# Kernel optimization log

Measured on AMD Instinct MI355X. Metric: run time of the kernel, lower is better.

## Reference

```python
import jax, jax.numpy as jnp
import numpy as np
from jax import lax

N, C, M = 512, 81, 28
NMS_THRESH = 0.5
EPS = 1e-4


def setup_inputs() -> dict:
    key = jax.random.key(0)
    k1, k2, k3, k4 = jax.random.split(key, 4)
    return {
        "left_logits": jax.random.normal(k1, (N, C, M, M), dtype=jnp.float32),
        "right_logits": jax.random.normal(k2, (N, C, M, M), dtype=jnp.float32),
        "scores": jax.random.uniform(k3, (N,), dtype=jnp.float32),
        "labels": jax.random.randint(k4, (N,), 0, C),
    }


def mask_nms_keep(probs, scores, thresh):
    # probs: [N, M, M] float mask probabilities; greedy suppression in score order.
    n = probs.shape[0]
    order = jnp.argsort(-scores)
    P = probs[order].reshape(n, -1)                  # [N, M*M] sorted by score desc
    inter = P @ P.T                                   # pairwise sum(mask_i * mask_j)
    u = P.sum(-1)                                     # per-mask area (numerator mask only)
    iou = inter / (u[:, None] + EPS)                  # asymmetric IoU as in mask_iou()
    upper = jnp.triu(jnp.ones((n, n), dtype=bool), 1) # j > i

    def body(i, suppressed):
        sup_row = (~suppressed[i]) & upper[i] & (iou[i] >= thresh)
        return suppressed | sup_row

    suppressed = lax.fori_loop(0, n, body, jnp.zeros(n, dtype=bool))
    keep_sorted = ~suppressed
    # map back to original detection order
    return jnp.zeros(n, dtype=bool).at[order].set(keep_sorted)


def reference(left_logits, right_logits, scores, labels):
    idx = jnp.arange(left_logits.shape[0])
    # full-tensor sigmoid then per-class gather, as in the original module
    left_prob = jax.nn.sigmoid(left_logits)[idx, labels][:, None]    # [N,1,M,M]
    right_prob = jax.nn.sigmoid(right_logits)[idx, labels][:, None]  # [N,1,M,M]

    # filter_empty: both sides must have nonzero mask mass
    valid = (left_prob[:, 0].sum((-1, -2)) > 0) & (right_prob[:, 0].sum((-1, -2)) > 0)

    left_keep = mask_nms_keep(left_prob[:, 0], scores, NMS_THRESH)
    right_keep = mask_nms_keep(right_prob[:, 0], scores, NMS_THRESH)
    keep = valid & left_keep & right_keep  # intersection of left/right NMS keeps

    probs = jnp.stack([left_prob, right_prob], axis=0)  # [2,N,1,M,M]
    return probs, keep
```

## Files before the change

### kernel.cpp

```cpp
#include <hip/hip_runtime.h>
#include <math.h>

#define NDET 512
#define NCLS 81
#define MM   784
#define PROBS_ELEMS (2 * NDET * MM)
#define NMS_TH 0.5
#define EPS_D  1e-4
#define SDD 114


__global__ __launch_bounds__(256) void k12_fused(
    const float* __restrict__ left, const float* __restrict__ right,
    const float* __restrict__ scores, const int* __restrict__ labels,
    float* __restrict__ out, double* __restrict__ u, int* __restrict__ order) {
  if (blockIdx.x == 256) {
    __shared__ float sk[NDET];
    __shared__ int   si[NDET];
    int t = threadIdx.x;
    for (int e = t; e < NDET; e += 256) { sk[e] = scores[e]; si[e] = e; }
    __syncthreads();
    for (int k = 2; k <= NDET; k <<= 1) {
      for (int j = k >> 1; j > 0; j >>= 1) {
        for (int e = t; e < NDET; e += 256) {
          int p = e ^ j;
          if (p > e) {
            bool dir = ((e & k) == 0);
            float sa = sk[e], sb = sk[p];
            int ia = si[e], ib = si[p];
            bool aBeforeB = (sa > sb) || (sa == sb && ia < ib);
            bool doSwap = dir ? (!aBeforeB) : aBeforeB;
            if (doSwap) { sk[e] = sb; si[e] = ib; sk[p] = sa; si[p] = ia; }
          }
        }
        __syncthreads();
      }
    }
    for (int e = t; e < NDET; e += 256) order[e] = si[e];
    return;
  }

  int wv = threadIdx.x >> 6;
  int lane = threadIdx.x & 63;
  int m = (blockIdx.x << 2) | wv;
  int s = m >> 9;
  int n = m & 511;
  const float* src = (s == 0) ? left : right;
  int lab = labels[n];
  const float4* in4 = (const float4*)(src + ((size_t)n * NCLS + lab) * MM);
  float4* out4 = (float4*)(out + ((size_t)s * NDET + n) * MM);
  double local = 0.0;
  for (int i = lane; i < MM / 4; i += 64) {
    float4 v = in4[i];
    float4 r;
    r.x = 1.0f / (1.0f + expf(-v.x));
    r.y = 1.0f / (1.0f + expf(-v.y));
    r.z = 1.0f / (1.0f + expf(-v.z));
    r.w = 1.0f / (1.0f + expf(-v.w));
    out4[i] = r;
    local += (double)r.x + (double)r.y + (double)r.z + (double)r.w;
  }
#pragma unroll
  for (int off = 32; off > 0; off >>= 1)
    local += __shfl_down(local, off, 64);
  if (lane == 0) u[s * NDET + n] = local;
}

__global__ __launch_bounds__(256, 2) void k3_iou(
    const float* __restrict__ P,
    const double* __restrict__ u,
    const int* __restrict__ order,
    unsigned int* __restrict__ bits32) {
  int bi = blockIdx.x;
  int s = bi / 136;
  int tri = bi % 136;
  int ti = 0, rem = tri;
  while (rem >= 16 - ti) { rem -= 16 - ti; ti++; }
  int tj = ti + rem;

  __shared__ __align__(16) double arena[2 * 32 * SDD];
  double (*Asd)[SDD] = (double (*)[SDD])arena;
  double (*Bsd)[SDD] = (double (*)[SDD])(arena + 32 * SDD);
  double (*Cp)[33]   = (double (*)[33])arena;
  __shared__ int oi[32], oj[32];
  __shared__ double den05[32];
  __shared__ unsigned char pred[32][32];

  int t = threadIdx.x;
  if (t < 32) {
    int r = order[ti * 32 + t];
    oi[t] = r;
    den05[t] = 0.5 * (u[s * NDET + r] + EPS_D);
    oj[t] = order[tj * 32 + t];
  }
  __syncthreads();

  const float* Pside = P + (size_t)s * NDET * MM;

  const float4* gsrc[7];
  double* ldst[7];
#pragma unroll
  for (int i = 0; i < 7; i++) {
    int idx = t + 256 * i;
    int ab = (idx >= 896);
    int idc = ab ? (idx - 896) : idx;
    int r = idc / 28;
    int c4 = idc - r * 28;
    int o = ab ? oj[r] : oi[r];
    gsrc[i] = (const float4*)(Pside + (size_t)o * MM) + c4;
    ldst[i] = ab ? &Bsd[r][4 * c4] : &Asd[r][4 * c4];
  }

  float4 pf[7];
#pragma unroll
  for (int i = 0; i < 7; i++) pf[i] = gsrc[i][0];

  int wv = t >> 6;
  int lane = t & 63;
  int tx = lane & 7;
  int ty = (lane >> 3) & 7;
  int kb = 28 * wv;

  double acc[4][4];
#pragma unroll
  for (int i = 0; i < 4; i++)
#pragma unroll
    for (int j = 0; j < 4; j++) acc[i][j] = 0.0;

  for (int kc = 0; kc < 7; kc++) {
#pragma unroll
    for (int i = 0; i < 7; i++) {
      float4 v = pf[i];
      double2 d0; d0.x = (double)v.x; d0.y = (double)v.y;
      double2 d1; d1.x = (double)v.z; d1.y = (double)v.w;
      *(double2*)(ldst[i])     = d0;
      *(double2*)(ldst[i] + 2) = d1;
    }
    __syncthreads();
    if (kc < 6) {
#pragma unroll
      for (int i = 0; i < 7; i++) pf[i] = gsrc[i][(kc + 1) * 28];
    }
#pragma unroll
    for (int kp = 0; kp < 14; kp++) {
      double2 av[4], bv[4];
#pragma unroll
      for (int i = 0; i < 4; i++)
        av[i] = *(const double2*)&Asd[ty + 8 * i][kb + 2 * kp];
#pragma unroll
      for (int j = 0; j < 4; j++)
        bv[j] = *(const double2*)&Bsd[tx + 8 * j][kb + 2 * kp];
#pragma unroll
      for (int i = 0; i < 4; i++)
#pragma unroll
        for (int j = 0; j < 4; j++) {
          acc[i][j] = fma(av[i].x, bv[j].x, acc[i][j]);
          acc[i][j] = fma(av[i].y, bv[j].y, acc[i][j]);
        }
    }
    __syncthreads();
  }

  if (wv > 0) {
#pragma unroll
    for (int i = 0; i < 4; i++)
#pragma unroll
      for (int j = 0; j < 4; j++)
        Cp[(wv - 1) * 32 + ty + 8 * i][tx + 8 * j] = acc[i][j];
  }
  __syncthreads();
  if (wv == 0) {
#pragma unroll
    for (int i = 0; i < 4; i++) {
      int r = ty + 8 * i;
#pragma unroll
      for (int j = 0; j < 4; j++) {
        int c = tx + 8 * j;
        double v = acc[i][j] + Cp[0 * 32 + r][c] + Cp[1 * 32 + r][c] +
                   Cp[2 * 32 + r][c];
        pred[r][c] = (v >= den05[r]) ? 1 : 0;
      }
    }
  }
  __syncthreads();
  if (t < 32) {
    unsigned m = 0;
#pragma unroll
    for (int c = 0; c < 32; c++) m |= ((unsigned)pred[t][c]) << c;
    bits32[((size_t)s * NDET + ti * 32 + t) * 16 + tj] = m;
  }
}

__global__ __launch_bounds__(512) void k4_greedy(
    const unsigned long long* __restrict__ bits,
    const int* __restrict__ order,
    const double* __restrict__ u,
    float* __restrict__ outKeep) {
  __shared__ unsigned long long B[2 * NDET * 8];
  __shared__ unsigned char keepO[2 * NDET];
  int t = threadIdx.x;

  for (int e = t; e < 2 * NDET * 8; e += 512) {
    unsigned long long w = bits[e];
    int g = e & 7;
    int i = (e >> 3) & 511;
    int gi = i >> 6;
    if (g < gi) {
      w = 0ull;
    } else if (g == gi) {
      int li = i & 63;
      w = (li == 63) ? 0ull : (w & (~0ull << (li + 1)));
    }
    B[e] = w;
  }
  __syncthreads();

  int wv = t >> 6;
  int lane = t & 63;
  if (wv < 2) {
    int s = wv;
    const unsigned long long* Bside = B + (size_t)s * NDET * 8;
    unsigned long long S0 = 0, S1 = 0, S2 = 0, S3 = 0,
                       S4 = 0, S5 = 0, S6 = 0, S7 = 0;

#define GROUP(G, SG, ORS)                                              \
    for (int li = 0; li < 64; li++) {                                  \
      unsigned act = (unsigned)((SG >> li) & 1ull);                    \
      if (__builtin_amdgcn_readfirstlane(act) == 0) {                  \
        const unsigned long long* row = Bside + ((((G) << 6) | li) << 3); \
        ORS                                                            \
      }                                                                \
    }
    GROUP(0, S0, { S0 |= row[0]; S1 |= row[1]; S2 |= row[2]; S3 |= row[3];
                   S4 |= row[4]; S5 |= row[5]; S6 |= row[6]; S7 |= row[7]; })
    GROUP(1, S1, { S1 |= row[1]; S2 |= row[2]; S3 |= row[3];
                   S4 |= row[4]; S5 |= row[5]; S6 |= row[6]; S7 |= row[7]; })
    GROUP(2, S2, { S2 |= row[2]; S3 |= row[3];
                   S4 |= row[4]; S5 |= row[5]; S6 |= row[6]; S7 |= row[7]; })
    GROUP(3, S3, { S3 |= row[3];
                   S4 |= row[4]; S5 |= row[5]; S6 |= row[6]; S7 |= row[7]; })
    GROUP(4, S4, { S4 |= row[4]; S5 |= row[5]; S6 |= row[6]; S7 |= row[7]; })
    GROUP(5, S5, { S5 |= row[5]; S6 |= row[6]; S7 |= row[7]; })
    GROUP(6, S6, { S6 |= row[6]; S7 |= row[7]; })
    GROUP(7, S7, { S7 |= row[7]; })
#undef GROUP

    unsigned long long Sarr[8] = {S0, S1, S2, S3, S4, S5, S6, S7};
#pragma unroll
    for (int g = 0; g < 8; g++) {
      int c = (g << 6) | lane;
      keepO[s * NDET + order[c]] =
          (unsigned char)(((Sarr[g] >> lane) & 1ull) ^ 1ull);
    }
  }
  __syncthreads();

  if (t < NDET) {
    bool valid = (u[t] > 0.0) && (u[NDET + t] > 0.0);
    outKeep[t] = (valid && keepO[t] && keepO[NDET + t]) ? 1.0f : 0.0f;
  }
}

extern "C" void kernel_launch(void* const* d_in, const int* in_sizes, int n_in,
                              void* d_out, int out_size, void* d_ws, size_t ws_size,
                              hipStream_t stream) {
  const float* left   = (const float*)d_in[0];
  const float* right  = (const float*)d_in[1];
  const float* scores = (const float*)d_in[2];
  const int*   labels = (const int*)d_in[3];
  float* out = (float*)d_out;

  char* ws = (char*)d_ws;
  double* u                = (double*)(ws + 0);
  int* order               = (int*)(ws + 8192);
  unsigned int* bits32     = (unsigned int*)(ws + 16384);
  unsigned long long* bits = (unsigned long long*)(ws + 16384);

  k12_fused<<<257, 256, 0, stream>>>(left, right, scores, labels, out, u, order);
  k3_iou<<<272, 256, 0, stream>>>(out, u, order, bits32);
  k4_greedy<<<1, 512, 0, stream>>>(bits, order, u, out + PROBS_ELEMS);
}
```

Before: 281.7 us.

## Fuse greedy NMS into IoU kernel via last-block atomic counter; retile accumulators

```diff
diff --git a/kernel.cpp b/kernel.cpp
--- a/kernel.cpp
+++ b/kernel.cpp
@@ -13,11 +13,13 @@
 __global__ __launch_bounds__(256) void k12_fused(
     const float* __restrict__ left, const float* __restrict__ right,
     const float* __restrict__ scores, const int* __restrict__ labels,
-    float* __restrict__ out, double* __restrict__ u, int* __restrict__ order) {
+    float* __restrict__ out, double* __restrict__ u, int* __restrict__ order,
+    int* counter) {
   if (blockIdx.x == 256) {
     __shared__ float sk[NDET];
     __shared__ int   si[NDET];
     int t = threadIdx.x;
+    if (t == 0 && counter) *counter = 0;
     for (int e = t; e < NDET; e += 256) { sk[e] = scores[e]; si[e] = e; }
     __syncthreads();
     for (int k = 2; k <= NDET; k <<= 1) {
@@ -66,11 +68,20 @@
   if (lane == 0) u[s * NDET + n] = local;
 }
 
+__device__ __forceinline__ unsigned long long diagmask(unsigned long long w,
+                                                       int g, int gi, int li) {
+  if (g < gi) return 0ull;
+  if (g == gi) return (li == 63) ? 0ull : (w & (~0ull << (li + 1)));
+  return w;
+}
+
 __global__ __launch_bounds__(256, 2) void k3_iou(
     const float* __restrict__ P,
     const double* __restrict__ u,
     const int* __restrict__ order,
-    unsigned int* __restrict__ bits32) {
+    unsigned int* bits32,
+    float* __restrict__ outKeep,
+    int* counter, int fused) {
   int bi = blockIdx.x;
   int s = bi / 136;
   int tri = bi % 136;
@@ -78,13 +89,15 @@
   while (rem >= 16 - ti) { rem -= 16 - ti; ti++; }
   int tj = ti + rem;
 
-  __shared__ __align__(16) double arena[2 * 32 * SDD];
+  __shared__ __align__(16) double arena[8192];
   double (*Asd)[SDD] = (double (*)[SDD])arena;
   double (*Bsd)[SDD] = (double (*)[SDD])(arena + 32 * SDD);
   double (*Cp)[33]   = (double (*)[33])arena;
   __shared__ int oi[32], oj[32];
   __shared__ double den05[32];
   __shared__ unsigned char pred[32][32];
+  __shared__ unsigned char keepO[2 * NDET];
+  __shared__ int lastFlag;
 
   int t = threadIdx.x;
   if (t < 32) {
@@ -117,15 +130,16 @@
 
   int wv = t >> 6;
   int lane = t & 63;
-  int tx = lane & 7;
-  int ty = (lane >> 3) & 7;
-  int kb = 28 * wv;
-
-  double acc[4][4];
+  int tx = lane & 3;
+  int ty = (lane >> 2) & 7;
+  int kg = lane >> 5;
+  int kb = 14 * (wv * 2 + kg);
+
+  double acc[4][8];
 #pragma unroll
   for (int i = 0; i < 4; i++)
 #pragma unroll
-    for (int j = 0; j < 4; j++) acc[i][j] = 0.0;
+    for (int j = 0; j < 8; j++) acc[i][j] = 0.0;
 
   for (int kc = 0; kc < 7; kc++) {
 #pragma unroll
@@ -142,18 +156,18 @@
       for (int i = 0; i < 7; i++) pf[i] = gsrc[i][(kc + 1) * 28];
     }
 #pragma unroll
-    for (int kp = 0; kp < 14; kp++) {
-      double2 av[4], bv[4];
+    for (int kp = 0; kp < 7; kp++) {
+      double2 av[4], bv[8];
 #pragma unroll
       for (int i = 0; i < 4; i++)
         av[i] = *(const double2*)&Asd[ty + 8 * i][kb + 2 * kp];
 #pragma unroll
-      for (int j = 0; j < 4; j++)
-        bv[j] = *(const double2*)&Bsd[tx + 8 * j][kb + 2 * kp];
+      for (int j = 0; j < 8; j++)
+        bv[j] = *(const double2*)&Bsd[tx + 4 * j][kb + 2 * kp];
 #pragma unroll
       for (int i = 0; i < 4; i++)
 #pragma unroll
-        for (int j = 0; j < 4; j++) {
+        for (int j = 0; j < 8; j++) {
           acc[i][j] = fma(av[i].x, bv[j].x, acc[i][j]);
           acc[i][j] = fma(av[i].y, bv[j].y, acc[i][j]);
         }
@@ -161,21 +175,27 @@
     __syncthreads();
   }
 
-  if (wv > 0) {
+#pragma unroll
+  for (int i = 0; i < 4; i++)
+#pragma unroll
+    for (int j = 0; j < 8; j++)
+      acc[i][j] += __shfl_xor(acc[i][j], 32, 64);
+
+  if (wv > 0 && kg == 0) {
 #pragma unroll
     for (int i = 0; i < 4; i++)
 #pragma unroll
-      for (int j = 0; j < 4; j++)
-        Cp[(wv - 1) * 32 + ty + 8 * i][tx + 8 * j] = acc[i][j];
-  }
-  __syncthreads();
-  if (wv == 0) {
+      for (int j = 0; j < 8; j++)
+        Cp[(wv - 1) * 32 + ty + 8 * i][tx + 4 * j] = acc[i][j];
+  }
+  __syncthreads();
+  if (wv == 0 && kg == 0) {
 #pragma unroll
     for (int i = 0; i < 4; i++) {
       int r = ty + 8 * i;
 #pragma unroll
-      for (int j = 0; j < 4; j++) {
-        int c = tx + 8 * j;
+      for (int j = 0; j < 8; j++) {
+        int c = tx + 4 * j;
         double v = acc[i][j] + Cp[0 * 32 + r][c] + Cp[1 * 32 + r][c] +
                    Cp[2 * 32 + r][c];
         pred[r][c] = (v >= den05[r]) ? 1 : 0;
@@ -184,10 +204,77 @@
   }
   __syncthreads();
   if (t < 32) {
-    unsigned m = 0;
-#pragma unroll
-    for (int c = 0; c < 32; c++) m |= ((unsigned)pred[t][c]) << c;
-    bits32[((size_t)s * NDET + ti * 32 + t) * 16 + tj] = m;
+    unsigned mw = 0;
+#pragma unroll
+    for (int c = 0; c < 32; c++) mw |= ((unsigned)pred[t][c]) << c;
+    bits32[((size_t)s * NDET + ti * 32 + t) * 16 + tj] = mw;
+  }
+
+  if (!fused) return;
+
+  __syncthreads();
+  if (t == 0) {
+    __threadfence();
+    int old = atomicAdd(counter, 1);
+    lastFlag = (old == 271);
+  }
+  __syncthreads();
+  if (!lastFlag) return;
+  __threadfence();
+
+  const unsigned long long* bits = (const unsigned long long*)bits32;
+  unsigned long long* B2 = (unsigned long long*)arena;
+  for (int e = t; e < 2 * NDET * 8; e += 256) {
+    unsigned long long w = bits[e];
+    int g = e & 7;
+    int i = (e >> 3) & 511;
+    B2[e] = diagmask(w, g, i >> 6, i & 63);
+  }
+  __syncthreads();
+
+  int wv4 = t >> 6;
+  if (wv4 < 2) {
+    int sd = wv4;
+    const unsigned long long* Bside = B2 + (size_t)sd * NDET * 8;
+    unsigned long long S0 = 0, S1 = 0, S2 = 0, S3 = 0,
+                       S4 = 0, S5 = 0, S6 = 0, S7 = 0;
+
+#define GROUP2(G, SG, ORS)                                             \
+    for (int li = 0; li < 64; li++) {                                  \
+      unsigned act = (unsigned)((SG >> li) & 1ull);                    \
+      if (__builtin_amdgcn_readfirstlane(act) == 0) {                  \
+        const unsigned long long* row = Bside + ((((G) << 6) | li) << 3); \
+        ORS                                                            \
+      }                                                                \
+    }
+    GROUP2(0, S0, { S0 |= row[0]; S1 |= row[1]; S2 |= row[2]; S3 |= row[3];
+                    S4 |= row[4]; S5 |= row[5]; S6 |= row[6]; S7 |= row[7]; })
+    GROUP2(1, S1, { S1 |= row[1]; S2 |= row[2]; S3 |= row[3];
+                    S4 |= row[4]; S5 |= row[5]; S6 |= row[6]; S7 |= row[7]; })
+    GROUP2(2, S2, { S2 |= row[2]; S3 |= row[3];
+                    S4 |= row[4]; S5 |= row[5]; S6 |= row[6]; S7 |= row[7]; })
+    GROUP2(3, S3, { S3 |= row[3];
+                    S4 |= row[4]; S5 |= row[5]; S6 |= row[6]; S7 |= row[7]; })
+    GROUP2(4, S4, { S4 |= row[4]; S5 |= row[5]; S6 |= row[6]; S7 |= row[7]; })
+    GROUP2(5, S5, { S5 |= row[5]; S6 |= row[6]; S7 |= row[7]; })
+    GROUP2(6, S6, { S6 |= row[6]; S7 |= row[7]; })
+    GROUP2(7, S7, { S7 |= row[7]; })
+#undef GROUP2
+
+    unsigned long long Sarr[8] = {S0, S1, S2, S3, S4, S5, S6, S7};
+    int ln = t & 63;
+#pragma unroll
+    for (int g = 0; g < 8; g++) {
+      int c = (g << 6) | ln;
+      keepO[sd * NDET + order[c]] =
+          (unsigned char)(((Sarr[g] >> ln) & 1ull) ^ 1ull);
+    }
+  }
+  __syncthreads();
+
+  for (int e = t; e < NDET; e += 256) {
+    bool valid = (u[e] > 0.0) && (u[NDET + e] > 0.0);
+    outKeep[e] = (valid && keepO[e] && keepO[NDET + e]) ? 1.0f : 0.0f;
   }
 }
 
@@ -204,14 +291,7 @@
     unsigned long long w = bits[e];
     int g = e & 7;
     int i = (e >> 3) & 511;
-    int gi = i >> 6;
-    if (g < gi) {
-      w = 0ull;
-    } else if (g == gi) {
-      int li = i & 63;
-      w = (li == 63) ? 0ull : (w & (~0ull << (li + 1)));
-    }
-    B[e] = w;
+    B[e] = diagmask(w, g, i >> 6, i & 63);
   }
   __syncthreads();
 
@@ -276,7 +356,13 @@
   unsigned int* bits32     = (unsigned int*)(ws + 16384);
   unsigned long long* bits = (unsigned long long*)(ws + 16384);
 
-  k12_fused<<<257, 256, 0, stream>>>(left, right, scores, labels, out, u, order);
-  k3_iou<<<272, 256, 0, stream>>>(out, u, order, bits32);
-  k4_greedy<<<1, 512, 0, stream>>>(bits, order, u, out + PROBS_ELEMS);
-}
+  int fused = (ws_size >= (size_t)81928) ? 1 : 0;
+  int* counter = fused ? (int*)(ws + 81920) : nullptr;
+
+  k12_fused<<<257, 256, 0, stream>>>(left, right, scores, labels, out, u,
+                                     order, counter);
+  k3_iou<<<272, 256, 0, stream>>>(out, u, order, bits32, out + PROBS_ELEMS,
+                                  counter, fused);
+  if (!fused)
+    k4_greedy<<<1, 512, 0, stream>>>(bits, order, u, out + PROBS_ELEMS);
+}
```

After: 289.4 us. +2.7%, slower.
